# Performance work log

Measured on AMD Instinct MI355X. Metric: run time of the kernel, lower is better.

Reference implementation:

```python
import jax, jax.numpy as jnp
import numpy as np

S = 100   # n_pred_samples
B = 64    # batch
DIMS = [784, 512, 512, 10]


def setup_inputs() -> dict:
    key = jax.random.key(0)
    ks = jax.random.split(key, 16)
    d = {}
    d["inputs"] = jax.random.normal(ks[0], (B, DIMS[0]), dtype=jnp.float32)
    d["task_id"] = 0
    # variational params: means ~ 0.1*N(0,1), logvars constant -6 (as in module init)
    d["wm0"] = jax.random.normal(ks[1], (DIMS[0], DIMS[1])) * 0.1
    d["wv0"] = jnp.full((DIMS[0], DIMS[1]), -6.0, jnp.float32)
    d["bm0"] = jnp.full((DIMS[1],), 0.1, jnp.float32)
    d["bv0"] = jnp.full((DIMS[1],), -6.0, jnp.float32)
    d["wm1"] = jax.random.normal(ks[2], (DIMS[1], DIMS[2])) * 0.1
    d["wv1"] = jnp.full((DIMS[1], DIMS[2]), -6.0, jnp.float32)
    d["bm1"] = jnp.full((DIMS[2],), 0.1, jnp.float32)
    d["bv1"] = jnp.full((DIMS[2],), -6.0, jnp.float32)
    d["wml"] = jax.random.normal(ks[3], (DIMS[2], DIMS[3])) * 0.1
    d["wvl"] = jnp.full((DIMS[2], DIMS[3]), -6.0, jnp.float32)
    d["bml"] = jnp.full((DIMS[3],), 0.1, jnp.float32)
    d["bvl"] = jnp.full((DIMS[3],), -6.0, jnp.float32)
    # reparameterization noise (passed explicitly for determinism)
    d["we0"] = jax.random.normal(ks[4], (S, DIMS[0], DIMS[1]), dtype=jnp.float32)
    d["be0"] = jax.random.normal(ks[5], (S, 1, DIMS[1]), dtype=jnp.float32)
    d["we1"] = jax.random.normal(ks[6], (S, DIMS[1], DIMS[2]), dtype=jnp.float32)
    d["be1"] = jax.random.normal(ks[7], (S, 1, DIMS[2]), dtype=jnp.float32)
    d["wel"] = jax.random.normal(ks[8], (S, DIMS[2], DIMS[3]), dtype=jnp.float32)
    d["bel"] = jax.random.normal(ks[9], (S, 1, DIMS[3]), dtype=jnp.float32)
    return d


def _sample(eps, logvar, mean):
    # reparameterization: eps * exp(0.5*logvar) + mean
    return eps * jnp.exp(0.5 * logvar) + mean


def reference(inputs, task_id, wm0, wv0, bm0, bv0, wm1, wv1, bm1, bv1,
              wml, wvl, bml, bvl, we0, be0, we1, be1, wel, bel):
    # activations: [S, B, D]
    act = jnp.broadcast_to(inputs[None], (S,) + inputs.shape)
    # hidden layer 0
    W0 = _sample(we0, wv0, wm0)          # [S, D0, D1]
    b0 = _sample(be0, bv0, bm0)          # [S, 1, D1]
    act = jax.nn.relu(jnp.einsum('sbi,sio->sbo', act, W0) + b0)
    # hidden layer 1
    W1 = _sample(we1, wv1, wm1)
    b1 = _sample(be1, bv1, bm1)
    act = jax.nn.relu(jnp.einsum('sbi,sio->sbo', act, W1) + b1)
    # last (task-specific) layer: original does broadcast-mul + sum over dim 2,
    # which is exactly a batched matmul — expressed here as an einsum
    Wl = _sample(wel, wvl, wml)          # [S, D2, O]
    bl = _sample(bel, bvl, bml)          # [S, 1, O]
    logits = jnp.einsum('sbh,sho->sbo', act, Wl) + bl   # [S, B, O]
    return logits
```

## Files before the change

kernel.cpp:

```cpp
#include <hip/hip_runtime.h>
#include <hip/hip_bf16.h>


typedef __bf16 bf16x8 __attribute__((ext_vector_type(8)));
typedef float f32x4 __attribute__((ext_vector_type(4)));

#define NSAMP 100
#define BATCH 64
#define D0 784
#define D1 512
#define D2 512
#define DOUT 10
#define K0PAD 800
#define RSB 40

__device__ __forceinline__ unsigned short f2bf(float f) {
    __bf16 b = (__bf16)f;
    return __builtin_bit_cast(unsigned short, b);
}
__device__ __forceinline__ float bf_hi(unsigned int u) {
    return __builtin_bit_cast(float, u & 0xffff0000u);
}
__device__ __forceinline__ float bf_lo(unsigned int u) {
    return __builtin_bit_cast(float, u << 16);
}

union FragU { uint4 q; bf16x8 v; };

#define XB_N   (BATCH * K0PAD)
#define PS0_N  (D0 * D1)
#define PS1_N  (D1 * D2)
#define SGL_N  (D2 * DOUT)
#define B0_N   (NSAMP * D1)
#define B1_N   (NSAMP * D2)
#define BL_N   (NSAMP * DOUT)
#define PREP_TOTAL (XB_N + PS0_N + PS1_N + SGL_N + B0_N + B1_N + BL_N)

__global__ __launch_bounds__(256) void prep(
    const float* __restrict__ inputs,
    const float* __restrict__ wv0, const float* __restrict__ wm0,
    const float* __restrict__ wv1, const float* __restrict__ wm1,
    const float* __restrict__ wvl,
    const float* __restrict__ be0, const float* __restrict__ bv0, const float* __restrict__ bm0,
    const float* __restrict__ be1, const float* __restrict__ bv1, const float* __restrict__ bm1,
    const float* __restrict__ bel, const float* __restrict__ bvl, const float* __restrict__ bml,
    unsigned short* __restrict__ Xb,
    unsigned int* __restrict__ psm0, unsigned int* __restrict__ psm1,
    float* __restrict__ sigmal,
    float* __restrict__ bias0, float* __restrict__ bias1, float* __restrict__ biasl)
{
    int i = blockIdx.x * 256 + threadIdx.x;
    if (i < XB_N) {
        int m = i / K0PAD, k = i % K0PAD;
        float v = (k < D0) ? inputs[m * D0 + k] : 0.f;
        Xb[i] = f2bf(v);
        return;
    }
    i -= XB_N;
    if (i < PS0_N) {
        unsigned int sg = f2bf(__expf(0.5f * wv0[i]));
        unsigned int mn = f2bf(wm0[i]);
        psm0[i] = (sg << 16) | mn;
        return;
    }
    i -= PS0_N;
    if (i < PS1_N) {
        unsigned int sg = f2bf(__expf(0.5f * wv1[i]));
        unsigned int mn = f2bf(wm1[i]);
        psm1[i] = (sg << 16) | mn;
        return;
    }
    i -= PS1_N;
    if (i < SGL_N) { sigmal[i] = __expf(0.5f * wvl[i]); return; }
    i -= SGL_N;
    if (i < B0_N) { int n = i % D1; bias0[i] = fmaf(be0[i], __expf(0.5f * bv0[n]), bm0[n]); return; }
    i -= B0_N;
    if (i < B1_N) { int n = i % D2; bias1[i] = fmaf(be1[i], __expf(0.5f * bv1[n]), bm1[n]); return; }
    i -= B1_N;
    if (i < BL_N) { int o = i % DOUT; biasl[i] = fmaf(bel[i], __expf(0.5f * bvl[o]), bml[o]); return; }
}

__global__ __launch_bounds__(64) void gemm_wave(
    const unsigned short* __restrict__ A, int lda, long aStride,
    const float* __restrict__ eps, long eStride,
    const unsigned int* __restrict__ psm,
    int KT, int Kvalid,
    const float* __restrict__ bias,
    void* __restrict__ outp, int outBf16)
{
    __shared__ unsigned short smB[32 * RSB];

    const int bx = blockIdx.x;
    const int s  = bx >> 4;
    const int n0 = (bx & 15) << 5;
    const int l  = threadIdx.x;
    const int fr = l & 15, quad = l >> 4;
    const int kg = l >> 3;
    const int ng = l & 7;

    const unsigned short* aP = A + (long)s * aStride + (long)fr * lda + quad * 8;
    const float* eB        = eps + (long)s * eStride + n0 + 4 * ng;
    const unsigned int* pB = psm + n0 + 4 * ng;

    f32x4 acc[4][2] = {};

    float4 ea0[4], ea1[4];
    uint4  pa0[4], pa1[4], aa0[4], aa1[4];

    auto loadAll = [&](int kt, float4* ea, uint4* pa, uint4* aa) {
        const int kb = kt * 32;
#pragma unroll
        for (int mi = 0; mi < 4; ++mi)
            aa[mi] = *reinterpret_cast<const uint4*>(aP + (long)(mi * 16) * lda + kb);
#pragma unroll
        for (int j = 0; j < 4; ++j) {
            const int row = kb + 4 * kg + j;
            const bool ok = row < Kvalid;
            const long off = (long)(ok ? row : 0) * 512;
            float4 e = *reinterpret_cast<const float4*>(eB + off);
            uint4  p = *reinterpret_cast<const uint4*>(pB + off);
            if (!ok) { e = float4{0.f, 0.f, 0.f, 0.f}; p = uint4{0u, 0u, 0u, 0u}; }
            ea[j] = e; pa[j] = p;
        }
    };

    auto stage = [&](const float4* ea, const uint4* pa) {
        float w[4][4];
#pragma unroll
        for (int j = 0; j < 4; ++j) {
            w[j][0] = fmaf(ea[j].x, bf_hi(pa[j].x), bf_lo(pa[j].x));
            w[j][1] = fmaf(ea[j].y, bf_hi(pa[j].y), bf_lo(pa[j].y));
            w[j][2] = fmaf(ea[j].z, bf_hi(pa[j].z), bf_lo(pa[j].z));
            w[j][3] = fmaf(ea[j].w, bf_hi(pa[j].w), bf_lo(pa[j].w));
        }
#pragma unroll
        for (int i = 0; i < 4; ++i) {
            uint2 d;
            d.x = (unsigned)f2bf(w[0][i]) | ((unsigned)f2bf(w[1][i]) << 16);
            d.y = (unsigned)f2bf(w[2][i]) | ((unsigned)f2bf(w[3][i]) << 16);
            *reinterpret_cast<uint2*>(&smB[(4 * ng + i) * RSB + 4 * kg]) = d;
        }
    };

    auto compute = [&](const uint4* aa) {
        FragU bf0, bf1;
        bf0.q = *reinterpret_cast<const uint4*>(&smB[fr * RSB + quad * 8]);
        bf1.q = *reinterpret_cast<const uint4*>(&smB[(16 + fr) * RSB + quad * 8]);
#pragma unroll
        for (int mi = 0; mi < 4; ++mi) {
            FragU af; af.q = aa[mi];
            acc[mi][0] = __builtin_amdgcn_mfma_f32_16x16x32_bf16(af.v, bf0.v, acc[mi][0], 0, 0, 0);
            acc[mi][1] = __builtin_amdgcn_mfma_f32_16x16x32_bf16(af.v, bf1.v, acc[mi][1], 0, 0, 0);
        }
    };

    loadAll(0, ea0, pa0, aa0);
    int kt = 0;
    for (; kt + 2 <= KT; kt += 2) {
        loadAll(kt + 1, ea1, pa1, aa1);
        stage(ea0, pa0);
        compute(aa0);
        if (kt + 2 < KT) loadAll(kt + 2, ea0, pa0, aa0);
        stage(ea1, pa1);
        compute(aa1);
    }
    if (kt < KT) { stage(ea0, pa0); compute(aa0); }

    const float bv0v = bias[(long)s * 512 + n0 + fr];
    const float bv1v = bias[(long)s * 512 + n0 + 16 + fr];
    const long outBase = (long)s * BATCH * 512;
#pragma unroll
    for (int mi = 0; mi < 4; ++mi) {
#pragma unroll
        for (int ni = 0; ni < 2; ++ni) {
            const float bv = ni ? bv1v : bv0v;
            const int col = n0 + ni * 16 + fr;
#pragma unroll
            for (int r = 0; r < 4; ++r) {
                const int row = mi * 16 + quad * 4 + r;
                float v = fmaxf(acc[mi][ni][r] + bv, 0.f);
                const long idx = outBase + (long)row * 512 + col;
                if (outBf16) ((unsigned short*)outp)[idx] = f2bf(v);
                else         ((float*)outp)[idx] = v;
            }
        }
    }
}

__global__ __launch_bounds__(320) void last_layer(
    const float* __restrict__ act2,
    const float* __restrict__ wel,
    const float* __restrict__ sigmal,
    const float* __restrict__ wml,
    const float* __restrict__ biasl,
    float* __restrict__ out)
{
    __shared__ float smW[D2 * DOUT];
    const int s = blockIdx.x;
    const int t = threadIdx.x;
    const float* we = wel + (long)s * D2 * DOUT;
    for (int i = t; i < D2 * DOUT; i += 320)
        smW[i] = fmaf(we[i], sigmal[i], wml[i]);
    __syncthreads();

    const int m  = t / 5;
    const int op = t % 5;
    const float* a = act2 + ((long)s * BATCH + m) * D2;
    float acc0 = 0.f, acc1 = 0.f;
#pragma unroll 4
    for (int k = 0; k < D2; k += 4) {
        float4 av = *reinterpret_cast<const float4*>(a + k);
        acc0 = fmaf(av.x, smW[(k + 0) * DOUT + op], acc0);
        acc0 = fmaf(av.y, smW[(k + 1) * DOUT + op], acc0);
        acc0 = fmaf(av.z, smW[(k + 2) * DOUT + op], acc0);
        acc0 = fmaf(av.w, smW[(k + 3) * DOUT + op], acc0);
        acc1 = fmaf(av.x, smW[(k + 0) * DOUT + op + 5], acc1);
        acc1 = fmaf(av.y, smW[(k + 1) * DOUT + op + 5], acc1);
        acc1 = fmaf(av.z, smW[(k + 2) * DOUT + op + 5], acc1);
        acc1 = fmaf(av.w, smW[(k + 3) * DOUT + op + 5], acc1);
    }
    const long ob = ((long)s * BATCH + m) * DOUT;
    out[ob + op]     = acc0 + biasl[s * DOUT + op];
    out[ob + op + 5] = acc1 + biasl[s * DOUT + op + 5];
}

extern "C" void kernel_launch(void* const* d_in, const int* in_sizes, int n_in,
                              void* d_out, int out_size, void* d_ws, size_t ws_size,
                              hipStream_t stream)
{
    const float* inputs = (const float*)d_in[0];
    const float* wm0 = (const float*)d_in[2];
    const float* wv0 = (const float*)d_in[3];
    const float* bm0 = (const float*)d_in[4];
    const float* bv0 = (const float*)d_in[5];
    const float* wm1 = (const float*)d_in[6];
    const float* wv1 = (const float*)d_in[7];
    const float* bm1 = (const float*)d_in[8];
    const float* bv1 = (const float*)d_in[9];
    const float* wml = (const float*)d_in[10];
    const float* wvl = (const float*)d_in[11];
    const float* bml = (const float*)d_in[12];
    const float* bvl = (const float*)d_in[13];
    const float* we0 = (const float*)d_in[14];
    const float* be0 = (const float*)d_in[15];
    const float* we1 = (const float*)d_in[16];
    const float* be1 = (const float*)d_in[17];
    const float* wel = (const float*)d_in[18];
    const float* bel = (const float*)d_in[19];

    char* w = (char*)d_ws;
    unsigned short* Xb  = (unsigned short*)w; w += (size_t)XB_N * 2;
    unsigned int* psm0  = (unsigned int*)w;   w += (size_t)PS0_N * 4;
    unsigned int* psm1  = (unsigned int*)w;   w += (size_t)PS1_N * 4;
    float* sigmal = (float*)w; w += (size_t)SGL_N * 4;
    float* bias0  = (float*)w; w += (size_t)B0_N * 4;
    float* bias1  = (float*)w; w += (size_t)B1_N * 4;
    float* biasl  = (float*)w; w += (size_t)BL_N * 4;
    unsigned short* act1 = (unsigned short*)w; w += (size_t)NSAMP * BATCH * D1 * 2;
    float* act2 = (float*)w; w += (size_t)NSAMP * BATCH * D2 * 4;

    prep<<<dim3((PREP_TOTAL + 255) / 256), 256, 0, stream>>>(
        inputs, wv0, wm0, wv1, wm1, wvl,
        be0, bv0, bm0, be1, bv1, bm1, bel, bvl, bml,
        Xb, psm0, psm1, sigmal, bias0, bias1, biasl);

    gemm_wave<<<dim3(NSAMP * 16), 64, 0, stream>>>(
        Xb, K0PAD, 0L, we0, (long)D0 * D1, psm0,
        K0PAD / 32, D0, bias0, (void*)act1, 1);

    gemm_wave<<<dim3(NSAMP * 16), 64, 0, stream>>>(
        act1, D1, (long)BATCH * D1, we1, (long)D1 * D2, psm1,
        D1 / 32, D1, bias1, (void*)act2, 0);

    last_layer<<<dim3(NSAMP), 320, 0, stream>>>(
        act2, wel, sigmal, wml, biasl, (float*)d_out);
}
```

Measured before the change: 407.3 us.

## Split GEMM K-loop across two waves per block with LDS reduction

Each gemm_wave block now runs two wavefronts, each handling half of the K tiles with its own LDS staging buffer. Wave 1 writes its partial accumulators to shared memory, and wave 0 adds them before applying bias and ReLU and storing the output. This doubles the wavefronts in flight, aiming to hide the latency of the memory-bound epsilon and weight streaming. The cost is extra LDS use, a block barrier, and a reduction step.

New measurement: 402.4 us. No clear change (-1.2%).

```diff
diff --git a/kernel.cpp b/kernel.cpp
--- a/kernel.cpp
+++ b/kernel.cpp
@@ -13,6 +13,7 @@
 #define DOUT 10
 #define K0PAD 800
 #define RSB 40
+#define PS 72
 
 __device__ __forceinline__ unsigned short f2bf(float f) {
     __bf16 b = (__bf16)f;
@@ -80,7 +81,7 @@
     if (i < BL_N) { int o = i % DOUT; biasl[i] = fmaf(bel[i], __expf(0.5f * bvl[o]), bml[o]); return; }
 }
 
-__global__ __launch_bounds__(64) void gemm_wave(
+__global__ __launch_bounds__(128) void gemm_wave(
     const unsigned short* __restrict__ A, int lda, long aStride,
     const float* __restrict__ eps, long eStride,
     const unsigned int* __restrict__ psm,
@@ -88,12 +89,14 @@
     const float* __restrict__ bias,
     void* __restrict__ outp, int outBf16)
 {
-    __shared__ unsigned short smB[32 * RSB];
+    __shared__ unsigned short smB[2][32 * RSB];
+    __shared__ float psum[32 * PS];
 
     const int bx = blockIdx.x;
     const int s  = bx >> 4;
     const int n0 = (bx & 15) << 5;
-    const int l  = threadIdx.x;
+    const int l  = threadIdx.x & 63;
+    const int w  = threadIdx.x >> 6;
     const int fr = l & 15, quad = l >> 4;
     const int kg = l >> 3;
     const int ng = l & 7;
@@ -101,6 +104,7 @@
     const unsigned short* aP = A + (long)s * aStride + (long)fr * lda + quad * 8;
     const float* eB        = eps + (long)s * eStride + n0 + 4 * ng;
     const unsigned int* pB = psm + n0 + 4 * ng;
+    unsigned short* myB    = &smB[w][0];
 
     f32x4 acc[4][2] = {};
 
@@ -125,27 +129,27 @@
     };
 
     auto stage = [&](const float4* ea, const uint4* pa) {
-        float w[4][4];
+        float wv[4][4];
 #pragma unroll
         for (int j = 0; j < 4; ++j) {
-            w[j][0] = fmaf(ea[j].x, bf_hi(pa[j].x), bf_lo(pa[j].x));
-            w[j][1] = fmaf(ea[j].y, bf_hi(pa[j].y), bf_lo(pa[j].y));
-            w[j][2] = fmaf(ea[j].z, bf_hi(pa[j].z), bf_lo(pa[j].z));
-            w[j][3] = fmaf(ea[j].w, bf_hi(pa[j].w), bf_lo(pa[j].w));
+            wv[j][0] = fmaf(ea[j].x, bf_hi(pa[j].x), bf_lo(pa[j].x));
+            wv[j][1] = fmaf(ea[j].y, bf_hi(pa[j].y), bf_lo(pa[j].y));
+            wv[j][2] = fmaf(ea[j].z, bf_hi(pa[j].z), bf_lo(pa[j].z));
+            wv[j][3] = fmaf(ea[j].w, bf_hi(pa[j].w), bf_lo(pa[j].w));
         }
 #pragma unroll
         for (int i = 0; i < 4; ++i) {
             uint2 d;
-            d.x = (unsigned)f2bf(w[0][i]) | ((unsigned)f2bf(w[1][i]) << 16);
-            d.y = (unsigned)f2bf(w[2][i]) | ((unsigned)f2bf(w[3][i]) << 16);
-            *reinterpret_cast<uint2*>(&smB[(4 * ng + i) * RSB + 4 * kg]) = d;
+            d.x = (unsigned)f2bf(wv[0][i]) | ((unsigned)f2bf(wv[1][i]) << 16);
+            d.y = (unsigned)f2bf(wv[2][i]) | ((unsigned)f2bf(wv[3][i]) << 16);
+            *reinterpret_cast<uint2*>(&myB[(4 * ng + i) * RSB + 4 * kg]) = d;
         }
     };
 
     auto compute = [&](const uint4* aa) {
         FragU bf0, bf1;
-        bf0.q = *reinterpret_cast<const uint4*>(&smB[fr * RSB + quad * 8]);
-        bf1.q = *reinterpret_cast<const uint4*>(&smB[(16 + fr) * RSB + quad * 8]);
+        bf0.q = *reinterpret_cast<const uint4*>(&myB[fr * RSB + quad * 8]);
+        bf1.q = *reinterpret_cast<const uint4*>(&myB[(16 + fr) * RSB + quad * 8]);
 #pragma unroll
         for (int mi = 0; mi < 4; ++mi) {
             FragU af; af.q = aa[mi];
@@ -154,34 +158,55 @@
         }
     };
 
-    loadAll(0, ea0, pa0, aa0);
-    int kt = 0;
-    for (; kt + 2 <= KT; kt += 2) {
+    const int KTH = (KT + 1) >> 1;
+    const int tB  = w * KTH;
+    const int tE  = (tB + KTH < KT) ? (tB + KTH) : KT;
+
+    loadAll(tB, ea0, pa0, aa0);
+    int kt = tB;
+    for (; kt + 2 <= tE; kt += 2) {
         loadAll(kt + 1, ea1, pa1, aa1);
         stage(ea0, pa0);
         compute(aa0);
-        if (kt + 2 < KT) loadAll(kt + 2, ea0, pa0, aa0);
+        if (kt + 2 < tE) loadAll(kt + 2, ea0, pa0, aa0);
         stage(ea1, pa1);
         compute(aa1);
     }
-    if (kt < KT) { stage(ea0, pa0); compute(aa0); }
-
-    const float bv0v = bias[(long)s * 512 + n0 + fr];
-    const float bv1v = bias[(long)s * 512 + n0 + 16 + fr];
-    const long outBase = (long)s * BATCH * 512;
-#pragma unroll
-    for (int mi = 0; mi < 4; ++mi) {
-#pragma unroll
-        for (int ni = 0; ni < 2; ++ni) {
-            const float bv = ni ? bv1v : bv0v;
-            const int col = n0 + ni * 16 + fr;
-#pragma unroll
-            for (int r = 0; r < 4; ++r) {
-                const int row = mi * 16 + quad * 4 + r;
-                float v = fmaxf(acc[mi][ni][r] + bv, 0.f);
-                const long idx = outBase + (long)row * 512 + col;
-                if (outBf16) ((unsigned short*)outp)[idx] = f2bf(v);
-                else         ((float*)outp)[idx] = v;
+    if (kt < tE) { stage(ea0, pa0); compute(aa0); }
+
+    if (w == 1) {
+#pragma unroll
+        for (int mi = 0; mi < 4; ++mi) {
+#pragma unroll
+            for (int ni = 0; ni < 2; ++ni) {
+                const int col = ni * 16 + fr;
+                const int row = mi * 16 + quad * 4;
+                *reinterpret_cast<f32x4*>(&psum[col * PS + row]) = acc[mi][ni];
+            }
+        }
+    }
+    __syncthreads();
+    if (w == 0) {
+        const float bv0v = bias[(long)s * 512 + n0 + fr];
+        const float bv1v = bias[(long)s * 512 + n0 + 16 + fr];
+        const long outBase = (long)s * BATCH * 512;
+#pragma unroll
+        for (int mi = 0; mi < 4; ++mi) {
+#pragma unroll
+            for (int ni = 0; ni < 2; ++ni) {
+                const int col = ni * 16 + fr;
+                const int row4 = mi * 16 + quad * 4;
+                const f32x4 part = *reinterpret_cast<const f32x4*>(&psum[col * PS + row4]);
+                const float bv = ni ? bv1v : bv0v;
+                const int ocol = n0 + col;
+#pragma unroll
+                for (int r = 0; r < 4; ++r) {
+                    const int row = row4 + r;
+                    float v = fmaxf(acc[mi][ni][r] + part[r] + bv, 0.f);
+                    const long idx = outBase + (long)row * 512 + ocol;
+                    if (outBf16) ((unsigned short*)outp)[idx] = f2bf(v);
+                    else         ((float*)outp)[idx] = v;
+                }
             }
         }
     }
@@ -264,11 +289,11 @@
         be0, bv0, bm0, be1, bv1, bm1, bel, bvl, bml,
         Xb, psm0, psm1, sigmal, bias0, bias1, biasl);
 
-    gemm_wave<<<dim3(NSAMP * 16), 64, 0, stream>>>(
+    gemm_wave<<<dim3(NSAMP * 16), 128, 0, stream>>>(
         Xb, K0PAD, 0L, we0, (long)D0 * D1, psm0,
         K0PAD / 32, D0, bias0, (void*)act1, 1);
 
-    gemm_wave<<<dim3(NSAMP * 16), 64, 0, stream>>>(
+    gemm_wave<<<dim3(NSAMP * 16), 128, 0, stream>>>(
         act1, D1, (long)BATCH * D1, we1, (long)D1 * D2, psm1,
         D1 / 32, D1, bias1, (void*)act2, 0);
 
```

## Share packed weight params and input tile across four samples per block via LDS

Applied to the files above, without the earlier changes.

The one-wave-per-sample GEMM becomes a 256-thread block that handles four samples for the same output-column tile. The packed sigma/mean tile is loaded once into double-buffered LDS and shared by the four waves, and for layer 0 the shared input matrix is staged in LDS too. This cuts redundant global loads of the parameter tensor and input, at the cost of block-wide barriers each k-step and fewer blocks in the grid.

Measured after the change: 383.4 us. 5.9% less time.

```diff
diff --git a/kernel.cpp b/kernel.cpp
--- a/kernel.cpp
+++ b/kernel.cpp
@@ -13,6 +13,8 @@
 #define DOUT 10
 #define K0PAD 800
 #define RSB 40
+#define PSW 36
+#define ATS 40
 
 __device__ __forceinline__ unsigned short f2bf(float f) {
     __bf16 b = (__bf16)f;
@@ -26,6 +28,11 @@
 }
 
 union FragU { uint4 q; bf16x8 v; };
+
+__device__ __forceinline__ void lds_barrier() {
+    asm volatile("s_waitcnt lgkmcnt(0)" ::: "memory");
+    __builtin_amdgcn_s_barrier();
+}
 
 #define XB_N   (BATCH * K0PAD)
 #define PS0_N  (D0 * D1)
@@ -80,91 +87,136 @@
     if (i < BL_N) { int o = i % DOUT; biasl[i] = fmaf(bel[i], __expf(0.5f * bvl[o]), bml[o]); return; }
 }
 
-__global__ __launch_bounds__(64) void gemm_wave(
-    const unsigned short* __restrict__ A, int lda, long aStride,
+__global__ __launch_bounds__(256) void gemm_ms(
+    const unsigned short* __restrict__ A, int lda, long aStride, int aShared,
     const float* __restrict__ eps, long eStride,
     const unsigned int* __restrict__ psm,
     int KT, int Kvalid,
     const float* __restrict__ bias,
     void* __restrict__ outp, int outBf16)
 {
-    __shared__ unsigned short smB[32 * RSB];
+    __shared__ unsigned int   psmT[2][32 * PSW];
+    __shared__ unsigned short aT[2][64 * ATS];
+    __shared__ unsigned short smB[4][32 * RSB];
 
     const int bx = blockIdx.x;
-    const int s  = bx >> 4;
+    const int sg = bx >> 4;
     const int n0 = (bx & 15) << 5;
-    const int l  = threadIdx.x;
+    const int t  = threadIdx.x;
+    const int w  = t >> 6;
+    const int l  = t & 63;
+    const int s  = sg * 4 + w;
     const int fr = l & 15, quad = l >> 4;
     const int kg = l >> 3;
     const int ng = l & 7;
 
+    const int prow = t >> 3, pcol = (t & 7) << 2;
+    const int arow = t >> 2, acol = (t & 3) << 3;
+
     const unsigned short* aP = A + (long)s * aStride + (long)fr * lda + quad * 8;
-    const float* eB        = eps + (long)s * eStride + n0 + 4 * ng;
-    const unsigned int* pB = psm + n0 + 4 * ng;
+    const float* eB = eps + (long)s * eStride + n0 + 4 * ng;
 
     f32x4 acc[4][2] = {};
-
     float4 ea0[4], ea1[4];
-    uint4  pa0[4], pa1[4], aa0[4], aa1[4];
-
-    auto loadAll = [&](int kt, float4* ea, uint4* pa, uint4* aa) {
+    uint4  aa0[4], aa1[4];
+    uint4  pReg, aReg;
+
+    auto issueStage = [&](int kt) {
+        const int kb = kt * 32;
+        int pr = kb + prow; if (pr >= Kvalid) pr = Kvalid - 1;
+        pReg = *reinterpret_cast<const uint4*>(psm + (long)pr * 512 + n0 + pcol);
+        if (aShared)
+            aReg = *reinterpret_cast<const uint4*>(A + (long)arow * lda + kb + acol);
+    };
+    auto writeStage = [&](int buf) {
+        *reinterpret_cast<uint4*>(&psmT[buf][prow * PSW + pcol]) = pReg;
+        if (aShared)
+            *reinterpret_cast<uint4*>(&aT[buf][arow * ATS + acol]) = aReg;
+    };
+    auto issueA = [&](int kt, uint4* aa) {
         const int kb = kt * 32;
 #pragma unroll
         for (int mi = 0; mi < 4; ++mi)
             aa[mi] = *reinterpret_cast<const uint4*>(aP + (long)(mi * 16) * lda + kb);
+    };
+    auto issueEps = [&](int kt, float4* ea) {
+        const int kb = kt * 32;
 #pragma unroll
         for (int j = 0; j < 4; ++j) {
             const int row = kb + 4 * kg + j;
             const bool ok = row < Kvalid;
             const long off = (long)(ok ? row : 0) * 512;
             float4 e = *reinterpret_cast<const float4*>(eB + off);
-            uint4  p = *reinterpret_cast<const uint4*>(pB + off);
-            if (!ok) { e = float4{0.f, 0.f, 0.f, 0.f}; p = uint4{0u, 0u, 0u, 0u}; }
-            ea[j] = e; pa[j] = p;
-        }
-    };
-
-    auto stage = [&](const float4* ea, const uint4* pa) {
-        float w[4][4];
+            if (!ok) e = float4{0.f, 0.f, 0.f, 0.f};
+            ea[j] = e;
+        }
+    };
+
+    auto computeTile = [&](int buf, const float4* ea, const uint4* aa) {
+        uint4 p[4];
+#pragma unroll
+        for (int j = 0; j < 4; ++j)
+            p[j] = *reinterpret_cast<const uint4*>(&psmT[buf][(4 * kg + j) * PSW + 4 * ng]);
+        float wv[4][4];
 #pragma unroll
         for (int j = 0; j < 4; ++j) {
-            w[j][0] = fmaf(ea[j].x, bf_hi(pa[j].x), bf_lo(pa[j].x));
-            w[j][1] = fmaf(ea[j].y, bf_hi(pa[j].y), bf_lo(pa[j].y));
-            w[j][2] = fmaf(ea[j].z, bf_hi(pa[j].z), bf_lo(pa[j].z));
-            w[j][3] = fmaf(ea[j].w, bf_hi(pa[j].w), bf_lo(pa[j].w));
+            wv[j][0] = fmaf(ea[j].x, bf_hi(p[j].x), bf_lo(p[j].x));
+            wv[j][1] = fmaf(ea[j].y, bf_hi(p[j].y), bf_lo(p[j].y));
+            wv[j][2] = fmaf(ea[j].z, bf_hi(p[j].z), bf_lo(p[j].z));
+            wv[j][3] = fmaf(ea[j].w, bf_hi(p[j].w), bf_lo(p[j].w));
         }
 #pragma unroll
         for (int i = 0; i < 4; ++i) {
             uint2 d;
-            d.x = (unsigned)f2bf(w[0][i]) | ((unsigned)f2bf(w[1][i]) << 16);
-            d.y = (unsigned)f2bf(w[2][i]) | ((unsigned)f2bf(w[3][i]) << 16);
-            *reinterpret_cast<uint2*>(&smB[(4 * ng + i) * RSB + 4 * kg]) = d;
-        }
-    };
-
-    auto compute = [&](const uint4* aa) {
+            d.x = (unsigned)f2bf(wv[0][i]) | ((unsigned)f2bf(wv[1][i]) << 16);
+            d.y = (unsigned)f2bf(wv[2][i]) | ((unsigned)f2bf(wv[3][i]) << 16);
+            *reinterpret_cast<uint2*>(&smB[w][(4 * ng + i) * RSB + 4 * kg]) = d;
+        }
         FragU bf0, bf1;
-        bf0.q = *reinterpret_cast<const uint4*>(&smB[fr * RSB + quad * 8]);
-        bf1.q = *reinterpret_cast<const uint4*>(&smB[(16 + fr) * RSB + quad * 8]);
+        bf0.q = *reinterpret_cast<const uint4*>(&smB[w][fr * RSB + quad * 8]);
+        bf1.q = *reinterpret_cast<const uint4*>(&smB[w][(16 + fr) * RSB + quad * 8]);
 #pragma unroll
         for (int mi = 0; mi < 4; ++mi) {
-            FragU af; af.q = aa[mi];
+            FragU af;
+            if (aShared)
+                af.q = *reinterpret_cast<const uint4*>(&aT[buf][(fr + mi * 16) * ATS + quad * 8]);
+            else
+                af.q = aa[mi];
             acc[mi][0] = __builtin_amdgcn_mfma_f32_16x16x32_bf16(af.v, bf0.v, acc[mi][0], 0, 0, 0);
             acc[mi][1] = __builtin_amdgcn_mfma_f32_16x16x32_bf16(af.v, bf1.v, acc[mi][1], 0, 0, 0);
         }
     };
 
-    loadAll(0, ea0, pa0, aa0);
+    issueStage(0);
+    if (!aShared) issueA(0, aa0);
+    issueEps(0, ea0);
+    writeStage(0);
+    lds_barrier();
+
     int kt = 0;
-    for (; kt + 2 <= KT; kt += 2) {
-        loadAll(kt + 1, ea1, pa1, aa1);
-        stage(ea0, pa0);
-        compute(aa0);
-        if (kt + 2 < KT) loadAll(kt + 2, ea0, pa0, aa0);
-        stage(ea1, pa1);
-        compute(aa1);
-    }
-    if (kt < KT) { stage(ea0, pa0); compute(aa0); }
+    while (kt < KT) {
+        {
+            const int kn = (kt + 1 < KT) ? kt + 1 : kt;
+            issueStage(kn);
+            if (!aShared) issueA(kn, aa1);
+            issueEps(kn, ea1);
+            computeTile(0, ea0, aa0);
+            writeStage(1);
+            lds_barrier();
+        }
+        ++kt;
+        if (kt >= KT) break;
+        {
+            const int kn = (kt + 1 < KT) ? kt + 1 : kt;
+            issueStage(kn);
+            if (!aShared) issueA(kn, aa0);
+            issueEps(kn, ea0);
+            computeTile(1, ea1, aa1);
+            writeStage(0);
+            lds_barrier();
+        }
+        ++kt;
+    }
 
     const float bv0v = bias[(long)s * 512 + n0 + fr];
     const float bv1v = bias[(long)s * 512 + n0 + 16 + fr];
@@ -264,12 +316,12 @@
         be0, bv0, bm0, be1, bv1, bm1, bel, bvl, bml,
         Xb, psm0, psm1, sigmal, bias0, bias1, biasl);
 
-    gemm_wave<<<dim3(NSAMP * 16), 64, 0, stream>>>(
-        Xb, K0PAD, 0L, we0, (long)D0 * D1, psm0,
+    gemm_ms<<<dim3((NSAMP / 4) * 16), 256, 0, stream>>>(
+        Xb, K0PAD, 0L, 1, we0, (long)D0 * D1, psm0,
         K0PAD / 32, D0, bias0, (void*)act1, 1);
 
-    gemm_wave<<<dim3(NSAMP * 16), 64, 0, stream>>>(
-        act1, D1, (long)BATCH * D1, we1, (long)D1 * D2, psm1,
+    gemm_ms<<<dim3((NSAMP / 4) * 16), 256, 0, stream>>>(
+        act1, D1, (long)BATCH * D1, 0, we1, (long)D1 * D2, psm1,
         D1 / 32, D1, bias1, (void*)act2, 0);
 
     last_layer<<<dim3(NSAMP), 320, 0, stream>>>(
```

## Process four samples per GEMM block to reuse shared mean/sigma loads

Applied to the files above, without the earlier changes.

Each single-wave GEMM block now handles four posterior samples instead of one, so the packed mean/sigma tile and (for layer 0) the shared input tile are loaded once and reused across the four samples. A double-buffered shared-memory B tile alternates between samples, and the eps loads for the next K tile are issued ahead for all four samples. The grid shrinks fourfold to 400 single-wave blocks, which lowers occupancy on a large GPU and sharply raises register pressure (64 accumulator vectors plus many prefetch registers). That may cause spills or poor latency hiding.

After: 1.050 ms. 2.58x slower.

```diff
diff --git a/kernel.cpp b/kernel.cpp
--- a/kernel.cpp
+++ b/kernel.cpp
@@ -80,7 +80,8 @@
     if (i < BL_N) { int o = i % DOUT; biasl[i] = fmaf(bel[i], __expf(0.5f * bvl[o]), bml[o]); return; }
 }
 
-__global__ __launch_bounds__(64) void gemm_wave(
+template<int ASHARED>
+__global__ __launch_bounds__(64) void gemm_s4(
     const unsigned short* __restrict__ A, int lda, long aStride,
     const float* __restrict__ eps, long eStride,
     const unsigned int* __restrict__ psm,
@@ -88,100 +89,139 @@
     const float* __restrict__ bias,
     void* __restrict__ outp, int outBf16)
 {
-    __shared__ unsigned short smB[32 * RSB];
+    __shared__ unsigned short smB[2][32 * RSB];
 
     const int bx = blockIdx.x;
-    const int s  = bx >> 4;
+    const int sb = (bx >> 4) << 2;
     const int n0 = (bx & 15) << 5;
     const int l  = threadIdx.x;
     const int fr = l & 15, quad = l >> 4;
     const int kg = l >> 3;
     const int ng = l & 7;
 
-    const unsigned short* aP = A + (long)s * aStride + (long)fr * lda + quad * 8;
-    const float* eB        = eps + (long)s * eStride + n0 + 4 * ng;
+    const unsigned short* aP = A + (long)sb * aStride + (long)fr * lda + quad * 8;
+    const float* eB        = eps + (long)sb * eStride + n0 + 4 * ng;
     const unsigned int* pB = psm + n0 + 4 * ng;
 
-    f32x4 acc[4][2] = {};
-
-    float4 ea0[4], ea1[4];
-    uint4  pa0[4], pa1[4], aa0[4], aa1[4];
-
-    auto loadAll = [&](int kt, float4* ea, uint4* pa, uint4* aa) {
+    f32x4 acc[4][4][2] = {};
+    float4 eaA[4][4], eaB[4][4];
+    uint4  paA[4], paB[4];
+    uint4  aaS[4];
+    uint4  aaP[4][4];
+
+    auto issueEpsPA = [&](int kt, float4 (*ea)[4], uint4* pa) {
         const int kb = kt * 32;
-#pragma unroll
-        for (int mi = 0; mi < 4; ++mi)
-            aa[mi] = *reinterpret_cast<const uint4*>(aP + (long)(mi * 16) * lda + kb);
 #pragma unroll
         for (int j = 0; j < 4; ++j) {
             const int row = kb + 4 * kg + j;
             const bool ok = row < Kvalid;
             const long off = (long)(ok ? row : 0) * 512;
-            float4 e = *reinterpret_cast<const float4*>(eB + off);
-            uint4  p = *reinterpret_cast<const uint4*>(pB + off);
-            if (!ok) { e = float4{0.f, 0.f, 0.f, 0.f}; p = uint4{0u, 0u, 0u, 0u}; }
-            ea[j] = e; pa[j] = p;
-        }
-    };
-
-    auto stage = [&](const float4* ea, const uint4* pa) {
-        float w[4][4];
+            uint4 p = *reinterpret_cast<const uint4*>(pB + off);
+            if (!ok) p = uint4{0u, 0u, 0u, 0u};
+            pa[j] = p;
+#pragma unroll
+            for (int si = 0; si < 4; ++si) {
+                float4 e = *reinterpret_cast<const float4*>(eB + (long)si * eStride + off);
+                if (!ok) e = float4{0.f, 0.f, 0.f, 0.f};
+                ea[si][j] = e;
+            }
+        }
+    };
+
+    auto issueAA = [&](int kt) {
+        const int kb = kt * 32;
+        if constexpr (ASHARED) {
+#pragma unroll
+            for (int mi = 0; mi < 4; ++mi)
+                aaS[mi] = *reinterpret_cast<const uint4*>(aP + (long)(mi * 16) * lda + kb);
+        } else {
+#pragma unroll
+            for (int si = 0; si < 4; ++si)
+#pragma unroll
+                for (int mi = 0; mi < 4; ++mi)
+                    aaP[si][mi] = *reinterpret_cast<const uint4*>(
+                        aP + (long)si * aStride + (long)(mi * 16) * lda + kb);
+        }
+    };
+
+    auto stage = [&](const float4* ea, const uint4* pa, int buf) {
+        float wv[4][4];
 #pragma unroll
         for (int j = 0; j < 4; ++j) {
-            w[j][0] = fmaf(ea[j].x, bf_hi(pa[j].x), bf_lo(pa[j].x));
-            w[j][1] = fmaf(ea[j].y, bf_hi(pa[j].y), bf_lo(pa[j].y));
-            w[j][2] = fmaf(ea[j].z, bf_hi(pa[j].z), bf_lo(pa[j].z));
-            w[j][3] = fmaf(ea[j].w, bf_hi(pa[j].w), bf_lo(pa[j].w));
+            wv[j][0] = fmaf(ea[j].x, bf_hi(pa[j].x), bf_lo(pa[j].x));
+            wv[j][1] = fmaf(ea[j].y, bf_hi(pa[j].y), bf_lo(pa[j].y));
+            wv[j][2] = fmaf(ea[j].z, bf_hi(pa[j].z), bf_lo(pa[j].z));
+            wv[j][3] = fmaf(ea[j].w, bf_hi(pa[j].w), bf_lo(pa[j].w));
         }
 #pragma unroll
         for (int i = 0; i < 4; ++i) {
             uint2 d;
-            d.x = (unsigned)f2bf(w[0][i]) | ((unsigned)f2bf(w[1][i]) << 16);
-            d.y = (unsigned)f2bf(w[2][i]) | ((unsigned)f2bf(w[3][i]) << 16);
-            *reinterpret_cast<uint2*>(&smB[(4 * ng + i) * RSB + 4 * kg]) = d;
-        }
-    };
-
-    auto compute = [&](const uint4* aa) {
+            d.x = (unsigned)f2bf(wv[0][i]) | ((unsigned)f2bf(wv[1][i]) << 16);
+            d.y = (unsigned)f2bf(wv[2][i]) | ((unsigned)f2bf(wv[3][i]) << 16);
+            *reinterpret_cast<uint2*>(&smB[buf][(4 * ng + i) * RSB + 4 * kg]) = d;
+        }
+    };
+
+    auto compute = [&](int si, int buf) {
         FragU bf0, bf1;
-        bf0.q = *reinterpret_cast<const uint4*>(&smB[fr * RSB + quad * 8]);
-        bf1.q = *reinterpret_cast<const uint4*>(&smB[(16 + fr) * RSB + quad * 8]);
+        bf0.q = *reinterpret_cast<const uint4*>(&smB[buf][fr * RSB + quad * 8]);
+        bf1.q = *reinterpret_cast<const uint4*>(&smB[buf][(16 + fr) * RSB + quad * 8]);
 #pragma unroll
         for (int mi = 0; mi < 4; ++mi) {
-            FragU af; af.q = aa[mi];
-            acc[mi][0] = __builtin_amdgcn_mfma_f32_16x16x32_bf16(af.v, bf0.v, acc[mi][0], 0, 0, 0);
-            acc[mi][1] = __builtin_amdgcn_mfma_f32_16x16x32_bf16(af.v, bf1.v, acc[mi][1], 0, 0, 0);
-        }
-    };
-
-    loadAll(0, ea0, pa0, aa0);
+            FragU af;
+            if constexpr (ASHARED) af.q = aaS[mi];
+            else                   af.q = aaP[si][mi];
+            acc[si][mi][0] = __builtin_amdgcn_mfma_f32_16x16x32_bf16(af.v, bf0.v, acc[si][mi][0], 0, 0, 0);
+            acc[si][mi][1] = __builtin_amdgcn_mfma_f32_16x16x32_bf16(af.v, bf1.v, acc[si][mi][1], 0, 0, 0);
+        }
+    };
+
+    auto tileBody = [&](const float4 (*ea)[4], const uint4* pa) {
+#pragma unroll
+        for (int si = 0; si < 4; ++si) {
+            stage(ea[si], pa, si & 1);
+            compute(si, si & 1);
+        }
+    };
+
+    issueEpsPA(0, eaA, paA);
     int kt = 0;
-    for (; kt + 2 <= KT; kt += 2) {
-        loadAll(kt + 1, ea1, pa1, aa1);
-        stage(ea0, pa0);
-        compute(aa0);
-        if (kt + 2 < KT) loadAll(kt + 2, ea0, pa0, aa0);
-        stage(ea1, pa1);
-        compute(aa1);
-    }
-    if (kt < KT) { stage(ea0, pa0); compute(aa0); }
-
-    const float bv0v = bias[(long)s * 512 + n0 + fr];
-    const float bv1v = bias[(long)s * 512 + n0 + 16 + fr];
-    const long outBase = (long)s * BATCH * 512;
-#pragma unroll
-    for (int mi = 0; mi < 4; ++mi) {
-#pragma unroll
-        for (int ni = 0; ni < 2; ++ni) {
-            const float bv = ni ? bv1v : bv0v;
-            const int col = n0 + ni * 16 + fr;
-#pragma unroll
-            for (int r = 0; r < 4; ++r) {
-                const int row = mi * 16 + quad * 4 + r;
-                float v = fmaxf(acc[mi][ni][r] + bv, 0.f);
-                const long idx = outBase + (long)row * 512 + col;
-                if (outBf16) ((unsigned short*)outp)[idx] = f2bf(v);
-                else         ((float*)outp)[idx] = v;
+    while (kt < KT) {
+        {
+            if (kt + 1 < KT) issueEpsPA(kt + 1, eaB, paB);
+            issueAA(kt);
+            tileBody(eaA, paA);
+        }
+        ++kt;
+        if (kt >= KT) break;
+        {
+            if (kt + 1 < KT) issueEpsPA(kt + 1, eaA, paA);
+            issueAA(kt);
+            tileBody(eaB, paB);
+        }
+        ++kt;
+    }
+
+#pragma unroll
+    for (int si = 0; si < 4; ++si) {
+        const int s = sb + si;
+        const float bv0v = bias[(long)s * 512 + n0 + fr];
+        const float bv1v = bias[(long)s * 512 + n0 + 16 + fr];
+        const long outBase = (long)s * BATCH * 512;
+#pragma unroll
+        for (int mi = 0; mi < 4; ++mi) {
+#pragma unroll
+            for (int ni = 0; ni < 2; ++ni) {
+                const float bv = ni ? bv1v : bv0v;
+                const int col = n0 + ni * 16 + fr;
+#pragma unroll
+                for (int r = 0; r < 4; ++r) {
+                    const int row = mi * 16 + quad * 4 + r;
+                    float v = fmaxf(acc[si][mi][ni][r] + bv, 0.f);
+                    const long idx = outBase + (long)row * 512 + col;
+                    if (outBf16) ((unsigned short*)outp)[idx] = f2bf(v);
+                    else         ((float*)outp)[idx] = v;
+                }
             }
         }
     }
@@ -264,11 +304,11 @@
         be0, bv0, bm0, be1, bv1, bm1, bel, bvl, bml,
         Xb, psm0, psm1, sigmal, bias0, bias1, biasl);
 
-    gemm_wave<<<dim3(NSAMP * 16), 64, 0, stream>>>(
+    gemm_s4<1><<<dim3((NSAMP / 4) * 16), 64, 0, stream>>>(
         Xb, K0PAD, 0L, we0, (long)D0 * D1, psm0,
         K0PAD / 32, D0, bias0, (void*)act1, 1);
 
-    gemm_wave<<<dim3(NSAMP * 16), 64, 0, stream>>>(
+    gemm_s4<0><<<dim3((NSAMP / 4) * 16), 64, 0, stream>>>(
         act1, D1, (long)BATCH * D1, we1, (long)D1 * D2, psm1,
         D1 / 32, D1, bias1, (void*)act2, 0);
 
```
